# Optimization experiments

Hardware: AMD Instinct MI355X
Metric: run time of the kernel (lower is better)

The kernel has to match this reference:

```python
import jax, jax.numpy as jnp
import numpy as np
from functools import partial

IMG, P, C, E, DEPTH, H, FE, NCLS = 224, 16, 3, 768, 12, 12, 4, 1000
B = 32
NP = (IMG // P) ** 2          # 196 patches
N = NP + 1                    # +cls token
HD = E // H                   # 64
FF = FE * E                   # 3072
EPS = 1e-5


def setup_inputs() -> dict:
    key = jax.random.key(0)
    ks = iter(jax.random.split(key, 32))
    r = lambda shape, s=0.02: (jax.random.normal(next(ks), shape, jnp.float32) * s)
    inp = {
        "x": jax.random.normal(next(ks), (B, C, IMG, IMG), jnp.float32),
        "conv_w": r((E, C, P, P)),              # OIHW
        "conv_b": r((E,)),
        "cls_token": r((1, 1, E)),
        "pos_emb": r((1, N, E)),
        # stacked per-layer params; Linear weights stored as [in, out]
        "Wq": r((DEPTH, E, E)), "Wk": r((DEPTH, E, E)), "Wv": r((DEPTH, E, E)),
        "Wo": r((DEPTH, E, E)), "bo": r((DEPTH, E)),
        "ln1_g": jnp.ones((DEPTH, E)), "ln1_b": jnp.zeros((DEPTH, E)),
        "W1": r((DEPTH, E, FF)), "b1": r((DEPTH, FF)),
        "W2": r((DEPTH, FF, E)), "b2": r((DEPTH, E)),
        "ln2_g": jnp.ones((DEPTH, E)), "ln2_b": jnp.zeros((DEPTH, E)),
        "head_g": jnp.ones((E,)), "head_b": jnp.zeros((E,)),
        "head_W": r((E, NCLS)), "head_bias": r((NCLS,)),
    }
    return inp


def _ln(x, g, b):
    m = jnp.mean(x, axis=-1, keepdims=True)
    v = jnp.var(x, axis=-1, keepdims=True)
    return (x - m) * jax.lax.rsqrt(v + EPS) * g + b


def _block(h, p):
    Wq, Wk, Wv, Wo, bo, g1, bn1, W1, b1, W2, b2, g2, bn2 = p
    b, n, _ = h.shape
    q = (h @ Wq).reshape(b, n, H, HD)
    k = (h @ Wk).reshape(b, n, H, HD)
    v = (h @ Wv).reshape(b, n, H, HD)
    # NOTE: original scales by sqrt(embed_size), not sqrt(head_dim)
    energy = jnp.einsum("bqhd,bkhd->bhqk", q, k) / jnp.sqrt(jnp.float32(E))
    attn = jax.nn.softmax(energy, axis=-1)
    out = jnp.einsum("bhqk,bkhd->bqhd", attn, v).reshape(b, n, E)
    out = out @ Wo + bo
    x = _ln(out + h, g1, bn1)
    f = jax.nn.relu(x @ W1 + b1) @ W2 + b2
    return _ln(f + x, g2, bn2), None


def reference(x, conv_w, conv_b, cls_token, pos_emb, Wq, Wk, Wv, Wo, bo,
              ln1_g, ln1_b, W1, b1, W2, b2, ln2_g, ln2_b,
              head_g, head_b, head_W, head_bias):
    # patch embedding: strided conv == non-overlapping patch projection
    h = jax.lax.conv_general_dilated(
        x, conv_w, window_strides=(P, P), padding="VALID",
        dimension_numbers=("NCHW", "OIHW", "NCHW"))
    h = h + conv_b[None, :, None, None]
    h = h.reshape(B, E, NP).transpose(0, 2, 1)          # [B, NP, E]
    cls = jnp.broadcast_to(cls_token, (B, 1, E))
    h = jnp.concatenate([cls, h], axis=1) + pos_emb      # [B, N, E]
    params = (Wq, Wk, Wv, Wo, bo, ln1_g, ln1_b, W1, b1, W2, b2, ln2_g, ln2_b)
    h, _ = jax.lax.scan(_block, h, params)
    cls_final = h[:, 0]
    return _ln(cls_final, head_g, head_b) @ head_W + head_bias
```

## Files before the change

### kernel.cpp

```cpp
#include <hip/hip_runtime.h>

#define NTOK 197
#define BATCH 32
#define ROWS (BATCH*NTOK)
#define EMB 768
#define FFDIM 3072
#define NHEAD 12
#define HDIM 64
#define NPAD 224

typedef __bf16 bf16x8_t __attribute__((ext_vector_type(8)));
typedef float f32x4 __attribute__((ext_vector_type(4)));
typedef unsigned short u16;

__device__ __forceinline__ u16 f2b(float f) {
  union { float f; unsigned int u; } v; v.f = f;
  unsigned int r = v.u + 0x7fffu + ((v.u >> 16) & 1u);
  return (u16)(r >> 16);
}
__device__ __forceinline__ void gload16(const void* g, void* l) {
  __builtin_amdgcn_global_load_lds((const __attribute__((address_space(1))) void*)g,
                                   (__attribute__((address_space(3))) void*)l, 16, 0, 0);
}
__device__ __forceinline__ float wred_sum(float v) {
#pragma unroll
  for (int o = 32; o > 0; o >>= 1) v += __shfl_xor(v, o);
  return v;
}

__device__ __forceinline__ void xcd_swz(int& bx, int& by) {
  const int gx = gridDim.x;
  const int nwg = gx * gridDim.y;
  const int orig = by * gx + bx;
  const int q = nwg >> 3, r = nwg & 7;
  const int xcd = orig & 7, idx = orig >> 3;
  const int wg = (xcd < r ? xcd * (q + 1) : r * (q + 1) + (xcd - r) * q) + idx;
  by = wg / gx; bx = wg % gx;
}

template <bool HAS_BIAS, bool RELU, bool ADD_RES, bool OUT_BF16>
__global__ __launch_bounds__(256)
void gemm_bt(const u16* __restrict__ A, const u16* __restrict__ Bt, void* __restrict__ C,
             const float* __restrict__ bias, const float* __restrict__ res,
             int M, int N, int K) {
  __shared__ __align__(16) char lds[2][16384];
  const int tid = threadIdx.x;
  const int lane = tid & 63;
  const int wid = tid >> 6;
  const int wm = wid >> 1, wn = wid & 1;
  int bxs = blockIdx.x, bys = blockIdx.y;
  xcd_swz(bxs, bys);
  const int bm = bys * 128, bn = bxs * 128;
  const int r15 = lane & 15, khi = lane >> 4;

  f32x4 acc[4][4] = {};
  const int nk = K >> 5;

  auto stage = [&](int buf, int kt) {
    const int k0 = kt * 32 + khi * 8;
#pragma unroll
    for (int i = 0; i < 4; ++i) {
      int s = wid * 4 + i;
      char* ldst = &lds[buf][s * 1024];
      const u16* g;
      if (s < 8) {
        int row = bm + s * 16 + r15; if (row >= M) row = M - 1;
        g = A + (size_t)row * K + k0;
      } else {
        int row = bn + (s - 8) * 16 + r15;
        g = Bt + (size_t)row * K + k0;
      }
      gload16(g, ldst);
    }
  };

  stage(0, 0);
  __syncthreads();
  for (int kt = 0; kt < nk; ++kt) {
    const int cur = kt & 1;
    if (kt + 1 < nk) stage(cur ^ 1, kt + 1);
    bf16x8_t a[4], b[4];
#pragma unroll
    for (int mt = 0; mt < 4; ++mt)
      a[mt] = *(const bf16x8_t*)&lds[cur][(wm * 4 + mt) * 1024 + lane * 16];
#pragma unroll
    for (int nt = 0; nt < 4; ++nt)
      b[nt] = *(const bf16x8_t*)&lds[cur][8192 + (wn * 4 + nt) * 1024 + lane * 16];
#pragma unroll
    for (int mt = 0; mt < 4; ++mt)
#pragma unroll
      for (int nt = 0; nt < 4; ++nt)
        acc[mt][nt] = __builtin_amdgcn_mfma_f32_16x16x32_bf16(a[mt], b[nt], acc[mt][nt], 0, 0, 0);
    __syncthreads();
  }

#pragma unroll
  for (int mt = 0; mt < 4; ++mt) {
#pragma unroll
    for (int nt = 0; nt < 4; ++nt) {
      const int col = bn + wn * 64 + nt * 16 + r15;
      float bv = 0.f;
      if (HAS_BIAS) bv = bias[col];
#pragma unroll
      for (int j = 0; j < 4; ++j) {
        const int row = bm + wm * 64 + mt * 16 + khi * 4 + j;
        if (row < M) {
          float v = acc[mt][nt][j] + bv;
          if (ADD_RES) v += res[(size_t)row * N + col];
          if (RELU) v = v > 0.f ? v : 0.f;
          if (OUT_BF16) ((u16*)C)[(size_t)row * N + col] = f2b(v);
          else          ((float*)C)[(size_t)row * N + col] = v;
        }
      }
    }
  }
}

template <bool HAS_BIAS, bool RELU, bool OUT_BF16>
__global__ __launch_bounds__(512)
void gemm_bt2(const u16* __restrict__ A, const u16* __restrict__ Bt, void* __restrict__ C,
              const float* __restrict__ bias, int M, int N, int K) {
  __shared__ __align__(16) char lds[2][24576];
  const int tid = threadIdx.x;
  const int lane = tid & 63;
  const int wid = tid >> 6;
  const int wm = wid >> 1, wn = wid & 1;
  int bxs = blockIdx.x, bys = blockIdx.y;
  xcd_swz(bxs, bys);
  const int bm = bys * 256, bn = bxs * 128;
  const int r15 = lane & 15, khi = lane >> 4;

  f32x4 acc[4][4] = {};
  const int nk = K >> 5;

  auto stage = [&](int buf, int kt) {
    const int k0 = kt * 32 + khi * 8;
#pragma unroll
    for (int i = 0; i < 3; ++i) {
      int s = wid * 3 + i;
      char* ldst = &lds[buf][s * 1024];
      const u16* g;
      if (s < 16) {
        int row = bm + s * 16 + r15; if (row >= M) row = M - 1;
        g = A + (size_t)row * K + k0;
      } else {
        int row = bn + (s - 16) * 16 + r15;
        g = Bt + (size_t)row * K + k0;
      }
      gload16(g, ldst);
    }
  };

  stage(0, 0);
  __syncthreads();
  for (int kt = 0; kt < nk; ++kt) {
    const int cur = kt & 1;
    if (kt + 1 < nk) stage(cur ^ 1, kt + 1);
    bf16x8_t a[4], b[4];
#pragma unroll
    for (int mt = 0; mt < 4; ++mt)
      a[mt] = *(const bf16x8_t*)&lds[cur][(wm * 4 + mt) * 1024 + lane * 16];
#pragma unroll
    for (int nt = 0; nt < 4; ++nt)
      b[nt] = *(const bf16x8_t*)&lds[cur][16384 + (wn * 4 + nt) * 1024 + lane * 16];
#pragma unroll
    for (int mt = 0; mt < 4; ++mt)
#pragma unroll
      for (int nt = 0; nt < 4; ++nt)
        acc[mt][nt] = __builtin_amdgcn_mfma_f32_16x16x32_bf16(a[mt], b[nt], acc[mt][nt], 0, 0, 0);
    __syncthreads();
  }

#pragma unroll
  for (int mt = 0; mt < 4; ++mt) {
#pragma unroll
    for (int nt = 0; nt < 4; ++nt) {
      const int col = bn + wn * 64 + nt * 16 + r15;
      float bv = 0.f;
      if (HAS_BIAS) bv = bias[col];
#pragma unroll
      for (int j = 0; j < 4; ++j) {
        const int row = bm + wm * 64 + mt * 16 + khi * 4 + j;
        if (row < M) {
          float v = acc[mt][nt][j] + bv;
          if (RELU) v = v > 0.f ? v : 0.f;
          if (OUT_BF16) ((u16*)C)[(size_t)row * N + col] = f2b(v);
          else          ((float*)C)[(size_t)row * N + col] = v;
        }
      }
    }
  }
}

template <int NSK>
__global__ __launch_bounds__(256)
void gemm_bt_sk(const u16* __restrict__ A, const u16* __restrict__ Bt,
                float* __restrict__ P0, float* __restrict__ P1, float* __restrict__ P2,
                int M, int N, int K) {
  __shared__ __align__(16) char lds[2][16384];
  const int tid = threadIdx.x;
  const int lane = tid & 63;
  const int wid = tid >> 6;
  const int wm = wid >> 1, wn = wid & 1;
  int bxs = blockIdx.x, bys = blockIdx.y;
  xcd_swz(bxs, bys);
  const int bm = bys * 128, bn = bxs * 128;
  const int r15 = lane & 15, khi = lane >> 4;
  const int Kh = K / NSK;
  const int kbase = blockIdx.z * Kh;
  float* __restrict__ C = (blockIdx.z == 0) ? P0 : (blockIdx.z == 1 ? P1 : P2);

  f32x4 acc[4][4] = {};
  const int nk = Kh >> 5;

  auto stage = [&](int buf, int kt) {
    const int k0 = kbase + kt * 32 + khi * 8;
#pragma unroll
    for (int i = 0; i < 4; ++i) {
      int s = wid * 4 + i;
      char* ldst = &lds[buf][s * 1024];
      const u16* g;
      if (s < 8) {
        int row = bm + s * 16 + r15; if (row >= M) row = M - 1;
        g = A + (size_t)row * K + k0;
      } else {
        int row = bn + (s - 8) * 16 + r15;
        g = Bt + (size_t)row * K + k0;
      }
      gload16(g, ldst);
    }
  };

  stage(0, 0);
  __syncthreads();
  for (int kt = 0; kt < nk; ++kt) {
    const int cur = kt & 1;
    if (kt + 1 < nk) stage(cur ^ 1, kt + 1);
    bf16x8_t a[4], b[4];
#pragma unroll
    for (int mt = 0; mt < 4; ++mt)
      a[mt] = *(const bf16x8_t*)&lds[cur][(wm * 4 + mt) * 1024 + lane * 16];
#pragma unroll
    for (int nt = 0; nt < 4; ++nt)
      b[nt] = *(const bf16x8_t*)&lds[cur][8192 + (wn * 4 + nt) * 1024 + lane * 16];
#pragma unroll
    for (int mt = 0; mt < 4; ++mt)
#pragma unroll
      for (int nt = 0; nt < 4; ++nt)
        acc[mt][nt] = __builtin_amdgcn_mfma_f32_16x16x32_bf16(a[mt], b[nt], acc[mt][nt], 0, 0, 0);
    __syncthreads();
  }

#pragma unroll
  for (int mt = 0; mt < 4; ++mt) {
#pragma unroll
    for (int nt = 0; nt < 4; ++nt) {
      const int col = bn + wn * 64 + nt * 16 + r15;
#pragma unroll
      for (int j = 0; j < 4; ++j) {
        const int row = bm + wm * 64 + mt * 16 + khi * 4 + j;
        if (row < M) C[(size_t)row * N + col] = acc[mt][nt][j];
      }
    }
  }
}

__global__ __launch_bounds__(256)
void ln_red(const float* __restrict__ P0, const float* __restrict__ P1,
            const float* __restrict__ P2,
            const float* __restrict__ bias, const float* __restrict__ res,
            const float* __restrict__ g, const float* __restrict__ bv,
            float* __restrict__ o32, u16* __restrict__ obf) {
  const int row = blockIdx.x;
  const size_t base = (size_t)row * EMB;
  const int tid = threadIdx.x;
  float vv[3];
#pragma unroll
  for (int c = 0; c < 3; ++c) {
    int e = tid + c * 256;
    vv[c] = P0[base + e] + P1[base + e] + P2[base + e] + bias[e] + res[base + e];
  }
  float s = wred_sum(vv[0] + vv[1] + vv[2]);
  float s2 = wred_sum(vv[0] * vv[0] + vv[1] * vv[1] + vv[2] * vv[2]);
  __shared__ float rs[4], rq[4];
  const int wid = tid >> 6, lane = tid & 63;
  if (lane == 0) { rs[wid] = s; rq[wid] = s2; }
  __syncthreads();
  float S1 = rs[0] + rs[1] + rs[2] + rs[3];
  float S2 = rq[0] + rq[1] + rq[2] + rq[3];
  float mean = S1 * (1.0f / 768.0f);
  float var = S2 * (1.0f / 768.0f) - mean * mean;
  float inv = rsqrtf(var + 1e-5f);
#pragma unroll
  for (int c = 0; c < 3; ++c) {
    int e = tid + c * 256;
    float y = (vv[c] - mean) * inv * g[e] + bv[e];
    o32[base + e] = y;
    obf[base + e] = f2b(y);
  }
}

__global__ void prep_layer(const float* __restrict__ Wq, const float* __restrict__ Wk,
                           const float* __restrict__ Wv, const float* __restrict__ Wo,
                           const float* __restrict__ W1, const float* __restrict__ W2,
                           u16* __restrict__ qkvT, u16* __restrict__ woT,
                           u16* __restrict__ w1T, u16* __restrict__ w2T) {
  __shared__ float tbuf[32][33];
  const int t = blockIdx.x;
  const float* src; u16* dst; int K, N, nt, kt;
  if (t < 2304) {
    int seg = t / 576, r = t % 576;
    nt = r % 24; kt = r / 24; K = 768; N = 768;
    if (seg == 0)      { src = Wq; dst = qkvT; }
    else if (seg == 1) { src = Wk; dst = qkvT + (size_t)768 * 768; }
    else if (seg == 2) { src = Wv; dst = qkvT + (size_t)2 * 768 * 768; }
    else               { src = Wo; dst = woT; }
  } else if (t < 4608) {
    int r = t - 2304; nt = r % 96; kt = r / 96;
    K = 768; N = 3072; src = W1; dst = w1T;
  } else {
    int r = t - 4608; nt = r % 24; kt = r / 24;
    K = 3072; N = 768; src = W2; dst = w2T;
  }
  const int n0 = nt * 32, k0 = kt * 32;
  const int tx = threadIdx.x, ty = threadIdx.y;
#pragma unroll
  for (int i = 0; i < 4; ++i)
    tbuf[ty + i * 8][tx] = src[(size_t)(k0 + ty + i * 8) * N + n0 + tx];
  __syncthreads();
#pragma unroll
  for (int i = 0; i < 4; ++i)
    dst[(size_t)(n0 + ty + i * 8) * K + k0 + tx] = f2b(tbuf[tx][ty + i * 8]);
}

__global__ void convert_bf(const float* __restrict__ s, u16* __restrict__ d, size_t n) {
  size_t i = (size_t)blockIdx.x * 256 + threadIdx.x;
  if (i < n) d[i] = f2b(s[i]);
}

__global__ void transpose_head(const float* __restrict__ src, float* __restrict__ dst) {
  __shared__ float tbuf[32][33];
  const int n0 = blockIdx.x * 32, k0 = blockIdx.y * 32;
  const int tx = threadIdx.x, ty = threadIdx.y;
#pragma unroll
  for (int i = 0; i < 4; ++i) {
    int k = k0 + ty + i * 8, n = n0 + tx;
    if (n < 1000) tbuf[ty + i * 8][tx] = src[(size_t)k * 1000 + n];
  }
  __syncthreads();
#pragma unroll
  for (int i = 0; i < 4; ++i) {
    int n = n0 + ty + i * 8, k = k0 + tx;
    if (n < 1000) dst[(size_t)n * 768 + k] = tbuf[tx][ty + i * 8];
  }
}

__global__ void im2col(const float* __restrict__ x, u16* __restrict__ A) {
  size_t idx = (size_t)blockIdx.x * 256 + threadIdx.x;
  if (idx >= (size_t)6272 * 768) return;
  int k = (int)(idx % 768); size_t row = idx / 768;
  int b = (int)(row / 196), p = (int)(row % 196);
  int py = p / 14, px = p % 14;
  int c = k >> 8, rem = k & 255, ph = rem >> 4, pw = rem & 15;
  float v = x[(((size_t)b * 3 + c) * 224 + (py * 16 + ph)) * 224 + (px * 16 + pw)];
  A[idx] = f2b(v);
}

__global__ void assemble_h0(const float* __restrict__ pout, const float* __restrict__ cls,
                            const float* __restrict__ pos, float* __restrict__ h32,
                            u16* __restrict__ hbf) {
  const int row = blockIdx.x;
  const int b = row / NTOK, n = row % NTOK;
  for (int c = threadIdx.x; c < EMB; c += 256) {
    float v;
    if (n == 0) v = cls[c] + pos[c];
    else v = pout[((size_t)b * 196 + (n - 1)) * EMB + c] + pos[(size_t)n * EMB + c];
    h32[(size_t)row * EMB + c] = v;
    hbf[(size_t)row * EMB + c] = f2b(v);
  }
}

__global__ void build_vT(const u16* __restrict__ qkv, u16* __restrict__ vT) {
  size_t idx = (size_t)blockIdx.x * 256 + threadIdx.x;
  if (idx >= (size_t)384 * HDIM * NPAD) return;
  int nn = (int)(idx % NPAD); size_t t = idx / NPAD;
  int d = (int)(t % HDIM); int bh = (int)(t / HDIM);
  int b = bh / NHEAD, h = bh % NHEAD;
  u16 v = 0;
  if (nn < NTOK) v = qkv[((size_t)b * NTOK + nn) * 2304 + 1536 + h * HDIM + d];
  vT[idx] = v;
}

__global__ __launch_bounds__(256)
void attn_sm(const u16* __restrict__ qkv, u16* __restrict__ P) {
  __shared__ __align__(16) char kf[13 * 2 * 1024];
  __shared__ __align__(16) char qf[2 * 2 * 1024];
  __shared__ float S[32][NPAD];
  const int bh = blockIdx.y;
  const int b = bh / NHEAD, h = bh % NHEAD;
  const int qb = blockIdx.x;
  const int tid = threadIdx.x, lane = tid & 63, wid = tid >> 6;
  const int r15 = lane & 15, khi = lane >> 4;

  const u16* qbase = qkv + (size_t)b * NTOK * 2304 + h * HDIM;
  const u16* kbase = qbase + 768;

  for (int i = wid; i < 26; i += 4) {
    int sub = i >> 1, ks = i & 1;
    int row = sub * 16 + r15; if (row > 196) row = 196;
    gload16(kbase + (size_t)row * 2304 + ks * 32 + khi * 8, &kf[(size_t)i * 1024]);
  }
  {
    int i = wid;
    int sub = i >> 1, ks = i & 1;
    int row = qb * 32 + sub * 16 + r15; if (row > 196) row = 196;
    gload16(qbase + (size_t)row * 2304 + ks * 32 + khi * 8, &qf[(size_t)i * 1024]);
  }
  __syncthreads();

  const float scale = 0.03608439182435161f;
  for (int t = wid; t < 26; t += 4) {
    int qi = t / 13, ki = t % 13;
    f32x4 acc = {};
    bf16x8_t aq0 = *(const bf16x8_t*)&qf[(qi * 2 + 0) * 1024 + lane * 16];
    bf16x8_t aq1 = *(const bf16x8_t*)&qf[(qi * 2 + 1) * 1024 + lane * 16];
    bf16x8_t bk0 = *(const bf16x8_t*)&kf[(ki * 2 + 0) * 1024 + lane * 16];
    bf16x8_t bk1 = *(const bf16x8_t*)&kf[(ki * 2 + 1) * 1024 + lane * 16];
    acc = __builtin_amdgcn_mfma_f32_16x16x32_bf16(aq0, bk0, acc, 0, 0, 0);
    acc = __builtin_amdgcn_mfma_f32_16x16x32_bf16(aq1, bk1, acc, 0, 0, 0);
#pragma unroll
    for (int j = 0; j < 4; ++j) S[qi * 16 + khi * 4 + j][ki * 16 + r15] = acc[j] * scale;
  }
  __syncthreads();

  for (int i = 0; i < 8; ++i) {
    const int r = wid * 8 + i;
    const int q = qb * 32 + r;
    if (q > 196) continue;
    float vals[4]; float m = -1e30f;
#pragma unroll
    for (int c = 0; c < 4; ++c) {
      int col = lane + c * 64;
      float v = (col < NTOK) ? S[r][col] : -1e30f;
      vals[c] = v; m = fmaxf(m, v);
    }
#pragma unroll
    for (int o = 32; o > 0; o >>= 1) m = fmaxf(m, __shfl_xor(m, o));
    float s = 0.f;
#pragma unroll
    for (int c = 0; c < 4; ++c) { float e = __expf(vals[c] - m); vals[c] = e; s += e; }
    s = wred_sum(s);
    float inv = 1.f / s;
    u16* prow = P + ((size_t)bh * NTOK + q) * NPAD;
#pragma unroll
    for (int c = 0; c < 4; ++c) {
      int col = lane + c * 64;
      if (col < NPAD) prow[col] = f2b(vals[c] * inv);
    }
  }
}

__global__ __launch_bounds__(256)
void attn_pv(const u16* __restrict__ P, const u16* __restrict__ vT, u16* __restrict__ out) {
  __shared__ __align__(16) char lds[2][17 * 1024];
  const int bh = blockIdx.x;
  const int b = bh / NHEAD, h = bh % NHEAD;
  const int tid = threadIdx.x, lane = tid & 63, wid = tid >> 6;
  const int r15 = lane & 15, khi = lane >> 4;
  const u16* Pb = P + (size_t)bh * NTOK * NPAD;
  const u16* Vb = vT + (size_t)bh * HDIM * NPAD;

  f32x4 acc[4][4] = {};
  auto stage = [&](int buf, int kt) {
    for (int i = wid; i < 17; i += 4) {
      const u16* g;
      if (i < 13) { int row = i * 16 + r15; if (row > 196) row = 196;
                    g = Pb + (size_t)row * NPAD + kt * 32 + khi * 8; }
      else        { int row = (i - 13) * 16 + r15;
                    g = Vb + (size_t)row * NPAD + kt * 32 + khi * 8; }
      gload16(g, &lds[buf][i * 1024]);
    }
  };
  stage(0, 0);
  __syncthreads();
  for (int kt = 0; kt < 7; ++kt) {
    const int cur = kt & 1;
    if (kt + 1 < 7) stage(cur ^ 1, kt + 1);
    bf16x8_t bb[4];
#pragma unroll
    for (int di = 0; di < 4; ++di)
      bb[di] = *(const bf16x8_t*)&lds[cur][(13 + di) * 1024 + lane * 16];
#pragma unroll
    for (int s = 0; s < 4; ++s) {
      int qi = wid + s * 4;
      if (qi < 13) {
        bf16x8_t a = *(const bf16x8_t*)&lds[cur][qi * 1024 + lane * 16];
#pragma unroll
        for (int di = 0; di < 4; ++di)
          acc[s][di] = __builtin_amdgcn_mfma_f32_16x16x32_bf16(a, bb[di], acc[s][di], 0, 0, 0);
      }
    }
    __syncthreads();
  }
#pragma unroll
  for (int s = 0; s < 4; ++s) {
    int qi = wid + s * 4;
    if (qi >= 13) continue;
#pragma unroll
    for (int di = 0; di < 4; ++di) {
      int col = h * HDIM + di * 16 + r15;
#pragma unroll
      for (int j = 0; j < 4; ++j) {
        int q = qi * 16 + khi * 4 + j;
        if (q < NTOK) out[((size_t)b * NTOK + q) * EMB + col] = f2b(acc[s][di][j]);
      }
    }
  }
}

__global__ __launch_bounds__(256)
void ln_cls(const float* __restrict__ h32, const float* __restrict__ hg,
            const float* __restrict__ hb, float* __restrict__ cls_ln) {
  const int b = blockIdx.x;
  const float* xr = h32 + (size_t)b * NTOK * EMB;
  const int tid = threadIdx.x;
  float v0 = xr[tid], v1 = xr[tid + 256], v2 = xr[tid + 512];
  float s = wred_sum(v0 + v1 + v2);
  float s2 = wred_sum(v0 * v0 + v1 * v1 + v2 * v2);
  __shared__ float rs[4], rq[4];
  const int wid = tid >> 6, lane = tid & 63;
  if (lane == 0) { rs[wid] = s; rq[wid] = s2; }
  __syncthreads();
  float S1 = rs[0] + rs[1] + rs[2] + rs[3];
  float S2 = rq[0] + rq[1] + rq[2] + rq[3];
  float mean = S1 * (1.0f / 768.0f);
  float var = S2 * (1.0f / 768.0f) - mean * mean;
  float inv = rsqrtf(var + 1e-5f);
  cls_ln[(size_t)b * EMB + tid]       = (v0 - mean) * inv * hg[tid]       + hb[tid];
  cls_ln[(size_t)b * EMB + tid + 256] = (v1 - mean) * inv * hg[tid + 256] + hb[tid + 256];
  cls_ln[(size_t)b * EMB + tid + 512] = (v2 - mean) * inv * hg[tid + 512] + hb[tid + 512];
}

__global__ __launch_bounds__(256)
void head2(const float* __restrict__ cls_ln, const float* __restrict__ hWT,
           const float* __restrict__ bias, float* __restrict__ out) {
  __shared__ float t[EMB];
  const int b = blockIdx.y;
  const int tid = threadIdx.x, lane = tid & 63, wid = tid >> 6;
  t[tid] = cls_ln[(size_t)b * EMB + tid];
  t[tid + 256] = cls_ln[(size_t)b * EMB + tid + 256];
  t[tid + 512] = cls_ln[(size_t)b * EMB + tid + 512];
  __syncthreads();
  const int j = blockIdx.x * 4 + wid;
  const float* wr = hWT + (size_t)j * EMB;
  float a = 0.f;
#pragma unroll
  for (int i = 0; i < 12; ++i) {
    int e = lane + i * 64;
    a += t[e] * wr[e];
  }
  a = wred_sum(a);
  if (lane == 0) out[(size_t)b * 1000 + j] = a + bias[j];
}

extern "C" void kernel_launch(void* const* d_in, const int* in_sizes, int n_in,
                              void* d_out, int out_size, void* d_ws, size_t ws_size,
                              hipStream_t stream) {
  const float* x      = (const float*)d_in[0];
  const float* conv_w = (const float*)d_in[1];
  const float* conv_b = (const float*)d_in[2];
  const float* cls    = (const float*)d_in[3];
  const float* pos    = (const float*)d_in[4];
  const float* Wq     = (const float*)d_in[5];
  const float* Wk     = (const float*)d_in[6];
  const float* Wv     = (const float*)d_in[7];
  const float* Wo     = (const float*)d_in[8];
  const float* bo     = (const float*)d_in[9];
  const float* ln1g   = (const float*)d_in[10];
  const float* ln1b   = (const float*)d_in[11];
  const float* W1     = (const float*)d_in[12];
  const float* b1     = (const float*)d_in[13];
  const float* W2     = (const float*)d_in[14];
  const float* b2     = (const float*)d_in[15];
  const float* ln2g   = (const float*)d_in[16];
  const float* ln2b   = (const float*)d_in[17];
  const float* hg     = (const float*)d_in[18];
  const float* hb     = (const float*)d_in[19];
  const float* hW     = (const float*)d_in[20];
  const float* hbias  = (const float*)d_in[21];

  char* ws = (char*)d_ws;
  size_t off = 0;
  auto alloc = [&](size_t bytes) { void* p = ws + off; off += (bytes + 255) & ~(size_t)255; return p; };

  u16*   qkvT = (u16*)alloc((size_t)2304 * 768 * 2);
  u16*   woTl = (u16*)alloc((size_t)768 * 768 * 2);
  u16*   w1Tl = (u16*)alloc((size_t)3072 * 768 * 2);
  u16*   w2Tl = (u16*)alloc((size_t)768 * 3072 * 2);
  u16*   cw   = (u16*)alloc((size_t)768 * 768 * 2);
  float* h32  = (float*)alloc((size_t)ROWS * EMB * 4);
  u16*   hbf  = (u16*)alloc((size_t)ROWS * EMB * 2);
  u16*   qkv  = (u16*)alloc((size_t)ROWS * 2304 * 2);
  char*  big  = (char*)alloc((size_t)384 * NTOK * NPAD * 2 + (size_t)384 * HDIM * NPAD * 2);
  u16*   Pbuf = (u16*)big;
  u16*   vT   = (u16*)(big + (size_t)384 * NTOK * NPAD * 2);
  u16*   mid  = (u16*)big;
  float* pout = (float*)big;
  float* woP0 = (float*)big;
  float* woP1 = (float*)(big + (size_t)ROWS * EMB * 4);
  u16*   att  = (u16*)alloc((size_t)ROWS * EMB * 2);
  u16*   xbf  = att;
  float* ybuf = (float*)alloc((size_t)ROWS * EMB * 4);
  float* x32  = (float*)alloc((size_t)ROWS * EMB * 4);
  float* hWT  = (float*)alloc((size_t)1000 * EMB * 4);
  float* clsl = (float*)alloc((size_t)32 * EMB * 4);
  u16*   Apatch = qkv;
  float* woP2 = ybuf;
  float* f2P0 = (float*)qkv;
  float* f2P1 = ybuf;
  float* f2P2 = h32;

  if (off > ws_size) return;

  convert_bf<<<2304, 256, 0, stream>>>(conv_w, cw, (size_t)768 * 768);
  transpose_head<<<dim3(32, 24), dim3(32, 8), 0, stream>>>(hW, hWT);
  im2col<<<18816, 256, 0, stream>>>(x, Apatch);
  gemm_bt<true, false, false, false><<<dim3(6, 49), 256, 0, stream>>>(Apatch, cw, pout, conv_b, nullptr, 6272, 768, 768);
  assemble_h0<<<ROWS, 256, 0, stream>>>(pout, cls, pos, h32, hbf);

  for (int l = 0; l < 12; ++l) {
    const size_t wo = (size_t)l * 768 * 768;
    prep_layer<<<6912, dim3(32, 8), 0, stream>>>(
        Wq + wo, Wk + wo, Wv + wo, Wo + wo,
        W1 + (size_t)l * 768 * 3072, W2 + (size_t)l * 3072 * 768,
        qkvT, woTl, w1Tl, w2Tl);
    gemm_bt2<false, false, true><<<dim3(18, 25), 512, 0, stream>>>(
        hbf, qkvT, qkv, nullptr, ROWS, 2304, 768);
    build_vT<<<21504, 256, 0, stream>>>(qkv, vT);
    attn_sm<<<dim3(7, 384), 256, 0, stream>>>(qkv, Pbuf);
    attn_pv<<<384, 256, 0, stream>>>(Pbuf, vT, att);
    gemm_bt_sk<3><<<dim3(6, 50, 3), 256, 0, stream>>>(att, woTl, woP0, woP1, woP2, ROWS, 768, 768);
    ln_red<<<ROWS, 256, 0, stream>>>(woP0, woP1, woP2, bo + (size_t)l * 768, h32,
                                     ln1g + (size_t)l * 768, ln1b + (size_t)l * 768, x32, xbf);
    gemm_bt2<true, true, true><<<dim3(24, 25), 512, 0, stream>>>(
        xbf, w1Tl, mid, b1 + (size_t)l * 3072, ROWS, FFDIM, 768);
    gemm_bt_sk<3><<<dim3(6, 50, 3), 256, 0, stream>>>(mid, w2Tl, f2P0, f2P1, f2P2, ROWS, 768, FFDIM);
    ln_red<<<ROWS, 256, 0, stream>>>(f2P0, f2P1, f2P2, b2 + (size_t)l * 768, x32,
                                     ln2g + (size_t)l * 768, ln2b + (size_t)l * 768, h32, hbf);
  }

  ln_cls<<<32, 256, 0, stream>>>(h32, hg, hb, clsl);
  head2<<<dim3(250, 32), 256, 0, stream>>>(clsl, hWT, hbias, (float*)d_out);
}
```

Baseline: 3.955 ms.

## Fuse attention softmax and PV into one kernel, keep probabilities in LDS

Merges the QK^T+softmax kernel and the P·V kernel into a single kernel per (query block, batch-head). Softmax probabilities go straight into LDS in MFMA fragment layout instead of a padded global P buffer, which removes that global round trip and one launch per layer. Q and K fragments are now read directly from global memory rather than staged in LDS, and V^T tiles are loaded into LDS per block, so V is re-read by each of the 7 query blocks. The PV phase keeps only a small amount of MFMA work per wave.

```diff
diff --git a/kernel.cpp b/kernel.cpp
--- a/kernel.cpp
+++ b/kernel.cpp
@@ -392,10 +392,11 @@
 }
 
 __global__ __launch_bounds__(256)
-void attn_sm(const u16* __restrict__ qkv, u16* __restrict__ P) {
-  __shared__ __align__(16) char kf[13 * 2 * 1024];
-  __shared__ __align__(16) char qf[2 * 2 * 1024];
+void attn_fused(const u16* __restrict__ qkv, const u16* __restrict__ vT,
+                u16* __restrict__ out) {
   __shared__ float S[32][NPAD];
+  __shared__ __align__(16) char vf[28 * 1024];
+  __shared__ __align__(16) char pf[14 * 1024];
   const int bh = blockIdx.y;
   const int b = bh / NHEAD, h = bh % NHEAD;
   const int qb = blockIdx.x;
@@ -404,30 +405,25 @@
 
   const u16* qbase = qkv + (size_t)b * NTOK * 2304 + h * HDIM;
   const u16* kbase = qbase + 768;
-
-  for (int i = wid; i < 26; i += 4) {
-    int sub = i >> 1, ks = i & 1;
-    int row = sub * 16 + r15; if (row > 196) row = 196;
-    gload16(kbase + (size_t)row * 2304 + ks * 32 + khi * 8, &kf[(size_t)i * 1024]);
-  }
-  {
-    int i = wid;
-    int sub = i >> 1, ks = i & 1;
-    int row = qb * 32 + sub * 16 + r15; if (row > 196) row = 196;
-    gload16(qbase + (size_t)row * 2304 + ks * 32 + khi * 8, &qf[(size_t)i * 1024]);
-  }
-  __syncthreads();
+  const u16* Vb = vT + (size_t)bh * HDIM * NPAD;
+
+  for (int i = wid; i < 28; i += 4) {
+    int dsub = i / 7, ksl = i % 7;
+    gload16(Vb + (size_t)(dsub * 16 + r15) * NPAD + ksl * 32 + khi * 8, &vf[(size_t)i * 1024]);
+  }
 
   const float scale = 0.03608439182435161f;
   for (int t = wid; t < 26; t += 4) {
     int qi = t / 13, ki = t % 13;
+    int qrow = qb * 32 + qi * 16 + r15; if (qrow > 196) qrow = 196;
+    int krow = ki * 16 + r15;           if (krow > 196) krow = 196;
     f32x4 acc = {};
-    bf16x8_t aq0 = *(const bf16x8_t*)&qf[(qi * 2 + 0) * 1024 + lane * 16];
-    bf16x8_t aq1 = *(const bf16x8_t*)&qf[(qi * 2 + 1) * 1024 + lane * 16];
-    bf16x8_t bk0 = *(const bf16x8_t*)&kf[(ki * 2 + 0) * 1024 + lane * 16];
-    bf16x8_t bk1 = *(const bf16x8_t*)&kf[(ki * 2 + 1) * 1024 + lane * 16];
-    acc = __builtin_amdgcn_mfma_f32_16x16x32_bf16(aq0, bk0, acc, 0, 0, 0);
-    acc = __builtin_amdgcn_mfma_f32_16x16x32_bf16(aq1, bk1, acc, 0, 0, 0);
+#pragma unroll
+    for (int ks = 0; ks < 2; ++ks) {
+      bf16x8_t aq = *(const bf16x8_t*)(qbase + (size_t)qrow * 2304 + ks * 32 + khi * 8);
+      bf16x8_t bk = *(const bf16x8_t*)(kbase + (size_t)krow * 2304 + ks * 32 + khi * 8);
+      acc = __builtin_amdgcn_mfma_f32_16x16x32_bf16(aq, bk, acc, 0, 0, 0);
+    }
 #pragma unroll
     for (int j = 0; j < 4; ++j) S[qi * 16 + khi * 4 + j][ki * 16 + r15] = acc[j] * scale;
   }
@@ -451,69 +447,33 @@
     for (int c = 0; c < 4; ++c) { float e = __expf(vals[c] - m); vals[c] = e; s += e; }
     s = wred_sum(s);
     float inv = 1.f / s;
-    u16* prow = P + ((size_t)bh * NTOK + q) * NPAD;
+    const int qsub = r >> 4, lr = r & 15;
 #pragma unroll
     for (int c = 0; c < 4; ++c) {
       int col = lane + c * 64;
-      if (col < NPAD) prow[col] = f2b(vals[c] * inv);
-    }
-  }
-}
-
-__global__ __launch_bounds__(256)
-void attn_pv(const u16* __restrict__ P, const u16* __restrict__ vT, u16* __restrict__ out) {
-  __shared__ __align__(16) char lds[2][17 * 1024];
-  const int bh = blockIdx.x;
-  const int b = bh / NHEAD, h = bh % NHEAD;
-  const int tid = threadIdx.x, lane = tid & 63, wid = tid >> 6;
-  const int r15 = lane & 15, khi = lane >> 4;
-  const u16* Pb = P + (size_t)bh * NTOK * NPAD;
-  const u16* Vb = vT + (size_t)bh * HDIM * NPAD;
-
-  f32x4 acc[4][4] = {};
-  auto stage = [&](int buf, int kt) {
-    for (int i = wid; i < 17; i += 4) {
-      const u16* g;
-      if (i < 13) { int row = i * 16 + r15; if (row > 196) row = 196;
-                    g = Pb + (size_t)row * NPAD + kt * 32 + khi * 8; }
-      else        { int row = (i - 13) * 16 + r15;
-                    g = Vb + (size_t)row * NPAD + kt * 32 + khi * 8; }
-      gload16(g, &lds[buf][i * 1024]);
-    }
-  };
-  stage(0, 0);
-  __syncthreads();
-  for (int kt = 0; kt < 7; ++kt) {
-    const int cur = kt & 1;
-    if (kt + 1 < 7) stage(cur ^ 1, kt + 1);
-    bf16x8_t bb[4];
-#pragma unroll
-    for (int di = 0; di < 4; ++di)
-      bb[di] = *(const bf16x8_t*)&lds[cur][(13 + di) * 1024 + lane * 16];
-#pragma unroll
-    for (int s = 0; s < 4; ++s) {
-      int qi = wid + s * 4;
-      if (qi < 13) {
-        bf16x8_t a = *(const bf16x8_t*)&lds[cur][qi * 1024 + lane * 16];
-#pragma unroll
-        for (int di = 0; di < 4; ++di)
-          acc[s][di] = __builtin_amdgcn_mfma_f32_16x16x32_bf16(a, bb[di], acc[s][di], 0, 0, 0);
-      }
-    }
-    __syncthreads();
-  }
-#pragma unroll
-  for (int s = 0; s < 4; ++s) {
-    int qi = wid + s * 4;
-    if (qi >= 13) continue;
-#pragma unroll
-    for (int di = 0; di < 4; ++di) {
-      int col = h * HDIM + di * 16 + r15;
-#pragma unroll
-      for (int j = 0; j < 4; ++j) {
-        int q = qi * 16 + khi * 4 + j;
-        if (q < NTOK) out[((size_t)b * NTOK + q) * EMB + col] = f2b(acc[s][di][j]);
-      }
+      int ksl = col >> 5, lc = col & 31;
+      *(u16*)&pf[(size_t)(qsub * 7 + ksl) * 1024 + (lr + (lc >> 3) * 16) * 16 + (lc & 7) * 2]
+          = f2b(vals[c] * inv);
+    }
+  }
+  __syncthreads();
+
+  const int qsub = wid & 1, dbase = wid >> 1;
+#pragma unroll
+  for (int t = 0; t < 2; ++t) {
+    const int dsub = dbase + t * 2;
+    f32x4 acc = {};
+#pragma unroll
+    for (int ksl = 0; ksl < 7; ++ksl) {
+      bf16x8_t a  = *(const bf16x8_t*)&pf[(size_t)(qsub * 7 + ksl) * 1024 + lane * 16];
+      bf16x8_t bv = *(const bf16x8_t*)&vf[(size_t)(dsub * 7 + ksl) * 1024 + lane * 16];
+      acc = __builtin_amdgcn_mfma_f32_16x16x32_bf16(a, bv, acc, 0, 0, 0);
+    }
+    const int col = h * HDIM + dsub * 16 + r15;
+#pragma unroll
+    for (int j = 0; j < 4; ++j) {
+      int q = qb * 32 + qsub * 16 + khi * 4 + j;
+      if (q < NTOK) out[((size_t)b * NTOK + q) * EMB + col] = f2b(acc[j]);
     }
   }
 }
@@ -602,7 +562,6 @@
   u16*   hbf  = (u16*)alloc((size_t)ROWS * EMB * 2);
   u16*   qkv  = (u16*)alloc((size_t)ROWS * 2304 * 2);
   char*  big  = (char*)alloc((size_t)384 * NTOK * NPAD * 2 + (size_t)384 * HDIM * NPAD * 2);
-  u16*   Pbuf = (u16*)big;
   u16*   vT   = (u16*)(big + (size_t)384 * NTOK * NPAD * 2);
   u16*   mid  = (u16*)big;
   float* pout = (float*)big;
@@ -637,8 +596,7 @@
     gemm_bt2<false, false, true><<<dim3(18, 25), 512, 0, stream>>>(
         hbf, qkvT, qkv, nullptr, ROWS, 2304, 768);
     build_vT<<<21504, 256, 0, stream>>>(qkv, vT);
-    attn_sm<<<dim3(7, 384), 256, 0, stream>>>(qkv, Pbuf);
-    attn_pv<<<384, 256, 0, stream>>>(Pbuf, vT, att);
+    attn_fused<<<dim3(7, 384), 256, 0, stream>>>(qkv, vT, att);
     gemm_bt_sk<3><<<dim3(6, 50, 3), 256, 0, stream>>>(att, woTl, woP0, woP1, woP2, ROWS, 768, 768);
     ln_red<<<ROWS, 256, 0, stream>>>(woP0, woP1, woP2, bo + (size_t)l * 768, h32,
                                      ln1g + (size_t)l * 768, ln1b + (size_t)l * 768, x32, xbf);
```

After: 4.096 ms. 1.04x slower.
